# Kernel optimization log

Hardware: AMD Instinct MI355X
Metric: run time of the kernel (lower is better)

## Reference

```python
import jax, jax.numpy as jnp
import numpy as np

D_MODEL = 1024
N_HEADS = 16
D_K = D_MODEL // N_HEADS
SCALE = float(np.sqrt(D_K))


def setup_inputs() -> dict:
    key = jax.random.key(0)
    ks = jax.random.split(key, 11)
    B, L, D = 2, 2048, D_MODEL
    s = 1.0 / np.sqrt(D)
    inp = {
        "q": jax.random.normal(ks[0], (B, L, D), dtype=jnp.float32),
        "k": jax.random.normal(ks[1], (B, L, D), dtype=jnp.float32),
        "v": jax.random.normal(ks[2], (B, L, D), dtype=jnp.float32),
        "Wq": jax.random.normal(ks[3], (D, D), dtype=jnp.float32) * s,
        "bq": jnp.zeros((D,), dtype=jnp.float32),
        "Wk": jax.random.normal(ks[4], (D, D), dtype=jnp.float32) * s,
        "bk": jnp.zeros((D,), dtype=jnp.float32),
        "Wv": jax.random.normal(ks[5], (D, D), dtype=jnp.float32) * s,
        "bv": jnp.zeros((D,), dtype=jnp.float32),
        "Wo": jax.random.normal(ks[6], (D, D), dtype=jnp.float32) * s,
        "bo": jnp.zeros((D,), dtype=jnp.float32),
    }
    return inp


def reference(q, k, v, Wq, bq, Wk, bk, Wv, bv, Wo, bo):
    B, L, D = q.shape
    H, Dk = N_HEADS, D_K
    # projections: [B,L,D] -> [B,H,L,Dk]
    def proj(x, W, b):
        y = x @ W + b
        return y.reshape(B, -1, H, Dk).transpose(0, 2, 1, 3)
    qh = proj(q, Wq, bq)
    kh = proj(k, Wk, bk)
    vh = proj(v, Wv, bv)
    # scores [B,H,Lq,Lk]
    scores = jnp.einsum("bhqd,bhkd->bhqk", qh, kh) / SCALE
    attn = jax.nn.softmax(scores, axis=-1)  # dropout=0.0 -> identity
    out = jnp.einsum("bhqk,bhkd->bhqd", attn, vh)
    out = out.transpose(0, 2, 1, 3).reshape(B, -1, D)
    return out @ Wo + bo
```

## Files before the change

kernel.cpp:

```cpp
#include <hip/hip_runtime.h>
#include <hip/hip_bf16.h>
#include <stdint.h>
#include <stddef.h>

typedef unsigned short ushortT;
typedef __attribute__((ext_vector_type(8))) short bf16x8s;
typedef __attribute__((ext_vector_type(4))) float f32x4;
typedef __attribute__((ext_vector_type(16))) float f32x16;


__device__ __forceinline__ short f2bf(float f) {
  unsigned u = __float_as_uint(f);
  u += 0x7FFFu + ((u >> 16) & 1u);
  return (short)(u >> 16);
}

__device__ __forceinline__ bf16x8s cvt8(const float* src) {
  const float4* p = (const float4*)src;
  float4 a = p[0], b = p[1];
  bf16x8s r;
  r[0] = f2bf(a.x); r[1] = f2bf(a.y); r[2] = f2bf(a.z); r[3] = f2bf(a.w);
  r[4] = f2bf(b.x); r[5] = f2bf(b.y); r[6] = f2bf(b.z); r[7] = f2bf(b.w);
  return r;
}

__device__ __forceinline__ unsigned cvtpk_bf16(float lo, float hi) {
  unsigned r;
  asm("v_cvt_pk_bf16_f32 %0, %1, %2" : "=v"(r) : "v"(lo), "v"(hi));
  return r;
}

__device__ __forceinline__ void permlane32_swap(unsigned& a, unsigned& b) {
  asm("v_permlane32_swap_b32 %0, %1" : "+v"(a), "+v"(b));
}

__device__ __forceinline__ void load_lds16(const ushortT* g, ushortT* l) {
  __builtin_amdgcn_global_load_lds(
      (const __attribute__((address_space(1))) void*)(g),
      (__attribute__((address_space(3))) void*)(l), 16, 0, 0);
}

__global__ __launch_bounds__(256)
void prep(const float* __restrict__ q, const float* __restrict__ k,
          const float* __restrict__ v,
          const float* __restrict__ Wq, const float* __restrict__ Wk,
          const float* __restrict__ Wv, const float* __restrict__ Wo,
          ushortT* __restrict__ Qc, ushortT* __restrict__ Kc,
          ushortT* __restrict__ Vc, ushortT* __restrict__ Wt)
{
  const int z = blockIdx.z;
  if (z < 4) {
    if (blockIdx.x >= 1024) return;
    __shared__ __align__(16) ushortT t[32][33];
    const float* W = (z == 0) ? Wq : (z == 1) ? Wk : (z == 2) ? Wv : Wo;
    ushortT* dst = Wt + (size_t)z * 1024 * 1024;
    const int x = (blockIdx.x & 31) * 32, y = (blockIdx.x >> 5) * 32;
    const int tx = threadIdx.x & 31, ty = threadIdx.x >> 5;
#pragma unroll
    for (int i = ty; i < 32; i += 8)
      t[i][tx] = (ushortT)f2bf(W[(size_t)(y + i) * 1024 + x + tx]);
    __syncthreads();
#pragma unroll
    for (int i = ty; i < 32; i += 8)
      dst[(size_t)(x + i) * 1024 + y + tx] = t[tx][i];
  } else {
    const float* src = (z == 4) ? q : (z == 5) ? k : v;
    ushortT* dst = (z == 4) ? Qc : (z == 5) ? Kc : Vc;
    const size_t i8 = ((size_t)blockIdx.x * 256 + threadIdx.x) * 8;
    *(bf16x8s*)(dst + i8) = cvt8(src + i8);
  }
}

__device__ __forceinline__ void gemm_core_128(
    const ushortT* __restrict__ A, const ushortT* __restrict__ Bt,
    int K, ushortT* As, ushortT* Bs, f32x4 (&acc)[4][4], int m0, int n0)
{
  const int tid  = threadIdx.x;
  const int wave = tid >> 6, lane = tid & 63;
  const int wm = (wave & 1) << 6;
  const int wn = (wave >> 1) << 6;
  const int lr = lane & 15;
  const int lk = (lane >> 4) << 3;

#pragma unroll
  for (int mi = 0; mi < 4; ++mi)
#pragma unroll
    for (int ni = 0; ni < 4; ++ni)
      acc[mi][ni] = (f32x4){0.f, 0.f, 0.f, 0.f};

  for (int k0 = 0; k0 < K; k0 += 32) {
    __syncthreads();
#pragma unroll
    for (int i = 0; i < 2; ++i) {
      const int cc  = tid + (i << 8);
      const int row = cc >> 2;
      const int ko  = (cc & 3) << 3;
      load_lds16(A  + (size_t)(m0 + row) * K + k0 + ko, As + cc * 8);
      load_lds16(Bt + (size_t)(n0 + row) * K + k0 + ko, Bs + cc * 8);
    }
    __syncthreads();

    bf16x8s af[4], bfr[4];
#pragma unroll
    for (int i = 0; i < 4; ++i)
      af[i] = *(const bf16x8s*)(As + (wm + i * 16 + lr) * 32 + lk);
#pragma unroll
    for (int i = 0; i < 4; ++i)
      bfr[i] = *(const bf16x8s*)(Bs + (wn + i * 16 + lr) * 32 + lk);

#pragma unroll
    for (int mi = 0; mi < 4; ++mi)
#pragma unroll
      for (int ni = 0; ni < 4; ++ni)
        acc[mi][ni] = __builtin_amdgcn_mfma_f32_16x16x32_bf16(
            af[mi], bfr[ni], acc[mi][ni], 0, 0, 0);
  }
}

__global__ __launch_bounds__(256)
void proj_gemm(const ushortT* __restrict__ Qc, const ushortT* __restrict__ Kc,
               const ushortT* __restrict__ Vc, const ushortT* __restrict__ WtAll,
               const float* __restrict__ bq, const float* __restrict__ bk,
               const float* __restrict__ bv,
               ushortT* __restrict__ Qh, ushortT* __restrict__ Kh,
               ushortT* __restrict__ Vt)
{
  __shared__ __align__(16) ushortT As[128 * 32];
  __shared__ __align__(16) ushortT Bs[128 * 32];
  const int which = blockIdx.z;
  const ushortT* A  = (which == 0) ? Qc : (which == 1) ? Kc : Vc;
  const ushortT* Bt = WtAll + (size_t)which * 1024 * 1024;
  const float* bias = (which == 0) ? bq : (which == 1) ? bk : bv;
  const int m0 = blockIdx.x * 128, n0 = blockIdx.y * 128;

  f32x4 acc[4][4];
  gemm_core_128(A, Bt, 1024, As, Bs, acc, m0, n0);

  const int lane = threadIdx.x & 63, wave = threadIdx.x >> 6;
  const int wm = (wave & 1) << 6, wn = (wave >> 1) << 6;
  const int lr = lane & 15, quad = lane >> 4;
  const float QSCALE = 0.18033688011112042f;

#pragma unroll
  for (int ni = 0; ni < 4; ++ni) {
    const int n = n0 + wn + ni * 16 + lr;
    const float bias_v = bias[n];
    const int h = n >> 6, d = n & 63;
#pragma unroll
    for (int mi = 0; mi < 4; ++mi) {
#pragma unroll
      for (int r = 0; r < 4; ++r) {
        const int m = m0 + wm + mi * 16 + quad * 4 + r;
        const int b = m >> 11, l = m & 2047;
        float val = acc[mi][ni][r] + bias_v;
        if (which == 0) val *= QSCALE;
        const ushortT o = (ushortT)f2bf(val);
        const size_t bh = (size_t)(b * 16 + h);
        if (which == 0)      Qh[(bh * 2048 + l) * 64 + d] = o;
        else if (which == 1) Kh[(bh * 2048 + l) * 64 + d] = o;
        else                 Vt[(bh * 64 + d) * 2048 + l] = o;
      }
    }
  }
}

__global__ __launch_bounds__(256)
void attn_kernel(const ushortT* __restrict__ Qh, const ushortT* __restrict__ Kh,
                 const ushortT* __restrict__ Vt, ushortT* __restrict__ Ob)
{
  const int b = blockIdx.z, h = blockIdx.y, qt = blockIdx.x;
  const int bh = b * 16 + h;
  const int wave = threadIdx.x >> 6, lane = threadIdx.x & 63;
  const int l31 = lane & 31, hi = lane >> 5, rk7 = l31 & 7;
  const int q0 = qt * 128 + wave * 32;

  const ushortT* Q = Qh + ((size_t)bh * 2048 + q0) * 64;
  const ushortT* K = Kh + (size_t)bh * 2048 * 64;
  const ushortT* V = Vt + (size_t)bh * 64 * 2048;

  __shared__ __align__(16) ushortT Ks[64 * 64];
  __shared__ __align__(16) ushortT Vs[64 * 64];
  __shared__ float fPs[4][32];
  float* fP = fPs[wave];

  bf16x8s qf[4];
#pragma unroll
  for (int s = 0; s < 4; ++s)
    qf[s] = *(const bf16x8s*)(Q + l31 * 64 + s * 16 + hi * 8);

  f32x16 o[2];
#pragma unroll
  for (int n = 0; n < 2; ++n)
#pragma unroll
    for (int r = 0; r < 16; ++r) o[n][r] = 0.f;
  float lsum = 0.f;

  const int tid = threadIdx.x;
  const int srow = tid >> 3;
  const int sc8  = (tid & 7) << 3;
  const int swz  = (((tid & 7) ^ (srow & 7)) << 3);
  const ushortT* Kg = K + (size_t)srow * 64 + sc8;
  const ushortT* Vg = V + (size_t)srow * 2048 + sc8;

  bf16x8s kch[2], vch[2];
  kch[0] = *(const bf16x8s*)(Kg);
  kch[1] = *(const bf16x8s*)(Kg + 32 * 64);
  vch[0] = *(const bf16x8s*)(Vg);
  vch[1] = *(const bf16x8s*)(Vg + 32 * 2048);

  for (int kt = 0; kt < 2048; kt += 64) {
    __syncthreads();
    *(bf16x8s*)(Ks + srow * 64 + swz)        = kch[0];
    *(bf16x8s*)(Ks + (srow + 32) * 64 + swz) = kch[1];
    *(bf16x8s*)(Vs + srow * 64 + swz)        = vch[0];
    *(bf16x8s*)(Vs + (srow + 32) * 64 + swz) = vch[1];
    __syncthreads();

    const int ktn = (kt + 64) & 2047;
    kch[0] = *(const bf16x8s*)(Kg + (size_t)ktn * 64);
    kch[1] = *(const bf16x8s*)(Kg + (size_t)(ktn + 32) * 64);
    vch[0] = *(const bf16x8s*)(Vg + ktn);
    vch[1] = *(const bf16x8s*)(Vg + 32 * 2048 + ktn);

    f32x16 sacc[2];
#pragma unroll
    for (int c = 0; c < 2; ++c)
#pragma unroll
      for (int r = 0; r < 16; ++r) sacc[c][r] = 0.f;

    __builtin_amdgcn_s_setprio(1);
#pragma unroll
    for (int s = 0; s < 4; ++s) {
      const int co = (((2 * s + hi) ^ rk7) << 3);
      const bf16x8s kf0 = *(const bf16x8s*)(Ks + l31 * 64 + co);
      const bf16x8s kf1 = *(const bf16x8s*)(Ks + (32 + l31) * 64 + co);
      sacc[0] = __builtin_amdgcn_mfma_f32_32x32x16_bf16(kf0, qf[s], sacc[0], 0, 0, 0);
      sacc[1] = __builtin_amdgcn_mfma_f32_32x32x16_bf16(kf1, qf[s], sacc[1], 0, 0, 0);
    }
    __builtin_amdgcn_s_setprio(0);

    bf16x8s pa[4];
#pragma unroll
    for (int c = 0; c < 2; ++c) {
      unsigned w[8];
#pragma unroll
      for (int i = 0; i < 8; ++i) {
        const float e0 = __builtin_amdgcn_exp2f(sacc[c][2 * i]);
        const float e1 = __builtin_amdgcn_exp2f(sacc[c][2 * i + 1]);
        lsum += e0 + e1;
        w[i] = cvtpk_bf16(e0, e1);
      }
      permlane32_swap(w[0], w[2]);
      permlane32_swap(w[1], w[3]);
      permlane32_swap(w[4], w[6]);
      permlane32_swap(w[5], w[7]);
      uint4 p0 = {w[0], w[1], w[2], w[3]};
      uint4 p1 = {w[4], w[5], w[6], w[7]};
      pa[2 * c]     = *(bf16x8s*)&p0;
      pa[2 * c + 1] = *(bf16x8s*)&p1;
    }

    __builtin_amdgcn_s_setprio(1);
#pragma unroll
    for (int s = 0; s < 4; ++s) {
      const int co = (((2 * s + hi) ^ rk7) << 3);
      const bf16x8s vf0 = *(const bf16x8s*)(Vs + l31 * 64 + co);
      const bf16x8s vf1 = *(const bf16x8s*)(Vs + (32 + l31) * 64 + co);
      o[0] = __builtin_amdgcn_mfma_f32_32x32x16_bf16(pa[s], vf0, o[0], 0, 0, 0);
      o[1] = __builtin_amdgcn_mfma_f32_32x32x16_bf16(pa[s], vf1, o[1], 0, 0, 0);
    }
    __builtin_amdgcn_s_setprio(0);
  }

  float s = lsum + __shfl_xor(lsum, 32);
  fP[l31] = 1.0f / s;
  asm volatile("s_waitcnt lgkmcnt(0)" ::: "memory");
  float invr[16];
#pragma unroll
  for (int r = 0; r < 16; ++r)
    invr[r] = fP[(r & 3) + 8 * (r >> 2) + 4 * hi];

#pragma unroll
  for (int n = 0; n < 2; ++n) {
    const int dcol = h * 64 + n * 32 + l31;
#pragma unroll
    for (int r = 0; r < 16; ++r) {
      const int l = q0 + (r & 3) + 8 * (r >> 2) + 4 * hi;
      Ob[((size_t)b * 2048 + l) * 1024 + dcol] =
          (ushortT)f2bf(o[n][r] * invr[r]);
    }
  }
}

__global__ __launch_bounds__(256)
void out_gemm(const ushortT* __restrict__ Ob, const ushortT* __restrict__ Wto,
              const float* __restrict__ bo, float* __restrict__ C)
{
  __shared__ __align__(16) ushortT As[128 * 32];
  __shared__ __align__(16) ushortT Bs[64 * 32];
  const int m0 = blockIdx.x * 128, n0 = blockIdx.y * 64;
  const int tid = threadIdx.x;
  const int wave = tid >> 6, lane = tid & 63;
  const int wm = (wave & 1) << 6;
  const int wn = (wave >> 1) << 5;
  const int lr = lane & 15, lk = (lane >> 4) << 3;

  f32x4 acc[4][2];
#pragma unroll
  for (int mi = 0; mi < 4; ++mi)
#pragma unroll
    for (int ni = 0; ni < 2; ++ni) acc[mi][ni] = (f32x4){0.f, 0.f, 0.f, 0.f};

  const int row = tid >> 2;
  const int ko  = (tid & 3) << 3;
  for (int k0 = 0; k0 < 1024; k0 += 32) {
    __syncthreads();
    load_lds16(Ob  + (size_t)(m0 + row) * 1024 + k0 + ko,      As + row * 32 + ko);
    load_lds16(Ob  + (size_t)(m0 + 64 + row) * 1024 + k0 + ko, As + (64 + row) * 32 + ko);
    load_lds16(Wto + (size_t)(n0 + row) * 1024 + k0 + ko,      Bs + row * 32 + ko);
    __syncthreads();

    bf16x8s af[4], bfr[2];
#pragma unroll
    for (int i = 0; i < 4; ++i)
      af[i] = *(const bf16x8s*)(As + (wm + i * 16 + lr) * 32 + lk);
#pragma unroll
    for (int i = 0; i < 2; ++i)
      bfr[i] = *(const bf16x8s*)(Bs + (wn + i * 16 + lr) * 32 + lk);

#pragma unroll
    for (int mi = 0; mi < 4; ++mi)
#pragma unroll
      for (int ni = 0; ni < 2; ++ni)
        acc[mi][ni] = __builtin_amdgcn_mfma_f32_16x16x32_bf16(
            af[mi], bfr[ni], acc[mi][ni], 0, 0, 0);
  }

  const int quad = lane >> 4;
#pragma unroll
  for (int ni = 0; ni < 2; ++ni) {
    const int n = n0 + wn + ni * 16 + lr;
    const float bias_v = bo[n];
#pragma unroll
    for (int mi = 0; mi < 4; ++mi) {
#pragma unroll
      for (int r = 0; r < 4; ++r) {
        const int m = m0 + wm + mi * 16 + quad * 4 + r;
        C[(size_t)m * 1024 + n] = acc[mi][ni][r] + bias_v;
      }
    }
  }
}

extern "C" void kernel_launch(void* const* d_in, const int* in_sizes, int n_in,
                              void* d_out, int out_size, void* d_ws, size_t ws_size,
                              hipStream_t stream) {
  const float* q  = (const float*)d_in[0];
  const float* k  = (const float*)d_in[1];
  const float* v  = (const float*)d_in[2];
  const float* Wq = (const float*)d_in[3];
  const float* bq = (const float*)d_in[4];
  const float* Wk = (const float*)d_in[5];
  const float* bk = (const float*)d_in[6];
  const float* Wv = (const float*)d_in[7];
  const float* bv = (const float*)d_in[8];
  const float* Wo = (const float*)d_in[9];
  const float* bo = (const float*)d_in[10];

  char* ws = (char*)d_ws;
  ushortT* Wt = (ushortT*)(ws);
  ushortT* Qh = (ushortT*)(ws + (size_t)(8  << 20));
  ushortT* Kh = (ushortT*)(ws + (size_t)(16 << 20));
  ushortT* Vt = (ushortT*)(ws + (size_t)(24 << 20));
  ushortT* Qc = (ushortT*)(ws + (size_t)(32 << 20));
  ushortT* Kc = (ushortT*)(ws + (size_t)(40 << 20));
  ushortT* Vc = (ushortT*)(ws + (size_t)(48 << 20));
  ushortT* Ob = Qc;

  prep<<<dim3(2048, 1, 7), 256, 0, stream>>>(q, k, v, Wq, Wk, Wv, Wo,
                                             Qc, Kc, Vc, Wt);
  proj_gemm<<<dim3(32, 8, 3), 256, 0, stream>>>(Qc, Kc, Vc, Wt, bq, bk, bv,
                                                Qh, Kh, Vt);
  attn_kernel<<<dim3(16, 16, 2), 256, 0, stream>>>(Qh, Kh, Vt, Ob);
  out_gemm<<<dim3(32, 16), 256, 0, stream>>>(Ob, Wt + (size_t)3 * 1024 * 1024,
                                             bo, (float*)d_out);
}
```

Measured before the change: 225.6 us.

## Use BK=64 tiles with XOR-swizzled LDS in projection and output GEMMs

Both the projection and output GEMMs now stage 64-wide K slices per iteration instead of 32, which halves the number of barrier pairs and loop trips. The LDS layout is XOR-swizzled by row so the 16-byte fragment reads avoid bank conflicts. The weight transpose in prep is also vectorized to float4 loads and ushort4 stores. In exchange, LDS use per block doubles, which may lower occupancy.

Measured after the change: 232.3 us. +3.0%, slower.

```diff
diff --git a/kernel.cpp b/kernel.cpp
--- a/kernel.cpp
+++ b/kernel.cpp
@@ -51,18 +51,22 @@
   const int z = blockIdx.z;
   if (z < 4) {
     if (blockIdx.x >= 1024) return;
-    __shared__ __align__(16) ushortT t[32][33];
+    __shared__ __align__(16) ushortT t[32][36];
     const float* W = (z == 0) ? Wq : (z == 1) ? Wk : (z == 2) ? Wv : Wo;
     ushortT* dst = Wt + (size_t)z * 1024 * 1024;
     const int x = (blockIdx.x & 31) * 32, y = (blockIdx.x >> 5) * 32;
-    const int tx = threadIdx.x & 31, ty = threadIdx.x >> 5;
-#pragma unroll
-    for (int i = ty; i < 32; i += 8)
-      t[i][tx] = (ushortT)f2bf(W[(size_t)(y + i) * 1024 + x + tx]);
-    __syncthreads();
-#pragma unroll
-    for (int i = ty; i < 32; i += 8)
-      dst[(size_t)(x + i) * 1024 + y + tx] = t[tx][i];
+    const int r  = threadIdx.x >> 3;
+    const int c4 = (threadIdx.x & 7) << 2;
+    const float4 wv = *(const float4*)(W + (size_t)(y + r) * 1024 + x + c4);
+    ushort4 tv;
+    tv.x = (ushortT)f2bf(wv.x); tv.y = (ushortT)f2bf(wv.y);
+    tv.z = (ushortT)f2bf(wv.z); tv.w = (ushortT)f2bf(wv.w);
+    *(ushort4*)&t[r][c4] = tv;
+    __syncthreads();
+    ushort4 o;
+    o.x = t[c4 + 0][r]; o.y = t[c4 + 1][r];
+    o.z = t[c4 + 2][r]; o.w = t[c4 + 3][r];
+    *(ushort4*)(dst + (size_t)(x + r) * 1024 + y + c4) = o;
   } else {
     const float* src = (z == 4) ? q : (z == 5) ? k : v;
     ushortT* dst = (z == 4) ? Qc : (z == 5) ? Kc : Vc;
@@ -71,7 +75,7 @@
   }
 }
 
-__device__ __forceinline__ void gemm_core_128(
+__device__ __forceinline__ void gemm_core_128_bk64(
     const ushortT* __restrict__ A, const ushortT* __restrict__ Bt,
     int K, ushortT* As, ushortT* Bs, f32x4 (&acc)[4][4], int m0, int n0)
 {
@@ -80,7 +84,7 @@
   const int wm = (wave & 1) << 6;
   const int wn = (wave >> 1) << 6;
   const int lr = lane & 15;
-  const int lk = (lane >> 4) << 3;
+  const int quad = (lane >> 4) & 3;
 
 #pragma unroll
   for (int mi = 0; mi < 4; ++mi)
@@ -88,32 +92,37 @@
     for (int ni = 0; ni < 4; ++ni)
       acc[mi][ni] = (f32x4){0.f, 0.f, 0.f, 0.f};
 
-  for (int k0 = 0; k0 < K; k0 += 32) {
-    __syncthreads();
-#pragma unroll
-    for (int i = 0; i < 2; ++i) {
+  for (int k0 = 0; k0 < K; k0 += 64) {
+    __syncthreads();
+#pragma unroll
+    for (int i = 0; i < 4; ++i) {
       const int cc  = tid + (i << 8);
-      const int row = cc >> 2;
-      const int ko  = (cc & 3) << 3;
-      load_lds16(A  + (size_t)(m0 + row) * K + k0 + ko, As + cc * 8);
-      load_lds16(Bt + (size_t)(n0 + row) * K + k0 + ko, Bs + cc * 8);
-    }
-    __syncthreads();
-
-    bf16x8s af[4], bfr[4];
-#pragma unroll
-    for (int i = 0; i < 4; ++i)
-      af[i] = *(const bf16x8s*)(As + (wm + i * 16 + lr) * 32 + lk);
-#pragma unroll
-    for (int i = 0; i < 4; ++i)
-      bfr[i] = *(const bf16x8s*)(Bs + (wn + i * 16 + lr) * 32 + lk);
-
-#pragma unroll
-    for (int mi = 0; mi < 4; ++mi)
-#pragma unroll
-      for (int ni = 0; ni < 4; ++ni)
-        acc[mi][ni] = __builtin_amdgcn_mfma_f32_16x16x32_bf16(
-            af[mi], bfr[ni], acc[mi][ni], 0, 0, 0);
+      const int row = cc >> 3;
+      const int pc  = cc & 7;
+      const int gko = ((pc ^ (row & 7)) << 3);
+      load_lds16(A  + (size_t)(m0 + row) * K + k0 + gko, As + cc * 8);
+      load_lds16(Bt + (size_t)(n0 + row) * K + k0 + gko, Bs + cc * 8);
+    }
+    __syncthreads();
+
+#pragma unroll
+    for (int kk = 0; kk < 2; ++kk) {
+      const int co = (((kk * 4 + quad) ^ (lr & 7)) << 3);
+      bf16x8s af[4], bfr[4];
+#pragma unroll
+      for (int i = 0; i < 4; ++i)
+        af[i] = *(const bf16x8s*)(As + (wm + i * 16 + lr) * 64 + co);
+#pragma unroll
+      for (int i = 0; i < 4; ++i)
+        bfr[i] = *(const bf16x8s*)(Bs + (wn + i * 16 + lr) * 64 + co);
+
+#pragma unroll
+      for (int mi = 0; mi < 4; ++mi)
+#pragma unroll
+        for (int ni = 0; ni < 4; ++ni)
+          acc[mi][ni] = __builtin_amdgcn_mfma_f32_16x16x32_bf16(
+              af[mi], bfr[ni], acc[mi][ni], 0, 0, 0);
+    }
   }
 }
 
@@ -125,8 +134,8 @@
                ushortT* __restrict__ Qh, ushortT* __restrict__ Kh,
                ushortT* __restrict__ Vt)
 {
-  __shared__ __align__(16) ushortT As[128 * 32];
-  __shared__ __align__(16) ushortT Bs[128 * 32];
+  __shared__ __align__(16) ushortT As[128 * 64];
+  __shared__ __align__(16) ushortT Bs[128 * 64];
   const int which = blockIdx.z;
   const ushortT* A  = (which == 0) ? Qc : (which == 1) ? Kc : Vc;
   const ushortT* Bt = WtAll + (size_t)which * 1024 * 1024;
@@ -134,7 +143,7 @@
   const int m0 = blockIdx.x * 128, n0 = blockIdx.y * 128;
 
   f32x4 acc[4][4];
-  gemm_core_128(A, Bt, 1024, As, Bs, acc, m0, n0);
+  gemm_core_128_bk64(A, Bt, 1024, As, Bs, acc, m0, n0);
 
   const int lane = threadIdx.x & 63, wave = threadIdx.x >> 6;
   const int wm = (wave & 1) << 6, wn = (wave >> 1) << 6;
@@ -296,14 +305,14 @@
 void out_gemm(const ushortT* __restrict__ Ob, const ushortT* __restrict__ Wto,
               const float* __restrict__ bo, float* __restrict__ C)
 {
-  __shared__ __align__(16) ushortT As[128 * 32];
-  __shared__ __align__(16) ushortT Bs[64 * 32];
+  __shared__ __align__(16) ushortT As[128 * 64];
+  __shared__ __align__(16) ushortT Bs[64 * 64];
   const int m0 = blockIdx.x * 128, n0 = blockIdx.y * 64;
   const int tid = threadIdx.x;
   const int wave = tid >> 6, lane = tid & 63;
   const int wm = (wave & 1) << 6;
   const int wn = (wave >> 1) << 5;
-  const int lr = lane & 15, lk = (lane >> 4) << 3;
+  const int lr = lane & 15, quad = (lane >> 4) & 3;
 
   f32x4 acc[4][2];
 #pragma unroll
@@ -311,32 +320,47 @@
 #pragma unroll
     for (int ni = 0; ni < 2; ++ni) acc[mi][ni] = (f32x4){0.f, 0.f, 0.f, 0.f};
 
-  const int row = tid >> 2;
-  const int ko  = (tid & 3) << 3;
-  for (int k0 = 0; k0 < 1024; k0 += 32) {
-    __syncthreads();
-    load_lds16(Ob  + (size_t)(m0 + row) * 1024 + k0 + ko,      As + row * 32 + ko);
-    load_lds16(Ob  + (size_t)(m0 + 64 + row) * 1024 + k0 + ko, As + (64 + row) * 32 + ko);
-    load_lds16(Wto + (size_t)(n0 + row) * 1024 + k0 + ko,      Bs + row * 32 + ko);
-    __syncthreads();
-
-    bf16x8s af[4], bfr[2];
-#pragma unroll
-    for (int i = 0; i < 4; ++i)
-      af[i] = *(const bf16x8s*)(As + (wm + i * 16 + lr) * 32 + lk);
-#pragma unroll
-    for (int i = 0; i < 2; ++i)
-      bfr[i] = *(const bf16x8s*)(Bs + (wn + i * 16 + lr) * 32 + lk);
-
-#pragma unroll
-    for (int mi = 0; mi < 4; ++mi)
-#pragma unroll
-      for (int ni = 0; ni < 2; ++ni)
-        acc[mi][ni] = __builtin_amdgcn_mfma_f32_16x16x32_bf16(
-            af[mi], bfr[ni], acc[mi][ni], 0, 0, 0);
-  }
-
-  const int quad = lane >> 4;
+  for (int k0 = 0; k0 < 1024; k0 += 64) {
+    __syncthreads();
+#pragma unroll
+    for (int i = 0; i < 4; ++i) {
+      const int cc  = tid + (i << 8);
+      const int row = cc >> 3;
+      const int pc  = cc & 7;
+      const int gko = ((pc ^ (row & 7)) << 3);
+      load_lds16(Ob + (size_t)(m0 + row) * 1024 + k0 + gko, As + cc * 8);
+    }
+#pragma unroll
+    for (int i = 0; i < 2; ++i) {
+      const int cc  = tid + (i << 8);
+      const int row = cc >> 3;
+      const int pc  = cc & 7;
+      const int gko = ((pc ^ (row & 7)) << 3);
+      load_lds16(Wto + (size_t)(n0 + row) * 1024 + k0 + gko, Bs + cc * 8);
+    }
+    __syncthreads();
+
+#pragma unroll
+    for (int kk = 0; kk < 2; ++kk) {
+      const int co = (((kk * 4 + quad) ^ (lr & 7)) << 3);
+      bf16x8s af[4], bfr[2];
+#pragma unroll
+      for (int i = 0; i < 4; ++i)
+        af[i] = *(const bf16x8s*)(As + (wm + i * 16 + lr) * 64 + co);
+#pragma unroll
+      for (int i = 0; i < 2; ++i)
+        bfr[i] = *(const bf16x8s*)(Bs + (wn + i * 16 + lr) * 64 + co);
+
+#pragma unroll
+      for (int mi = 0; mi < 4; ++mi)
+#pragma unroll
+        for (int ni = 0; ni < 2; ++ni)
+          acc[mi][ni] = __builtin_amdgcn_mfma_f32_16x16x32_bf16(
+              af[mi], bfr[ni], acc[mi][ni], 0, 0, 0);
+    }
+  }
+
+  const int quad4 = lane >> 4;
 #pragma unroll
   for (int ni = 0; ni < 2; ++ni) {
     const int n = n0 + wn + ni * 16 + lr;
@@ -345,7 +369,7 @@
     for (int mi = 0; mi < 4; ++mi) {
 #pragma unroll
       for (int r = 0; r < 4; ++r) {
-        const int m = m0 + wm + mi * 16 + quad * 4 + r;
+        const int m = m0 + wm + mi * 16 + quad4 * 4 + r;
         C[(size_t)m * 1024 + n] = acc[mi][ni][r] + bias_v;
       }
     }
```
